# Optimization experiments

Measured on AMD Instinct MI355X. Metric: run time of the kernel, lower is better.

Reference implementation:

```python
import jax, jax.numpy as jnp
import numpy as np

WORDS_CNT = 34835
EMBED_DIM = 512
NEG = -1e30  # stand-in for -inf that is safe under autodiff


def setup_inputs() -> dict:
    key = jax.random.key(0)
    k1, k2, k3, k4, k5 = jax.random.split(key, 5)
    B, Tt, Td = 2048, 30, 150
    title = jax.random.randint(k1, (B, Tt), 0, WORDS_CNT + 1, dtype=jnp.int64)
    desc = jax.random.randint(k2, (B, Td), 0, WORDS_CNT + 1, dtype=jnp.int64)
    t_len = jax.random.randint(k3, (B,), 0, Tt + 1, dtype=jnp.int64)
    d_len = jax.random.randint(k4, (B,), 0, Td + 1, dtype=jnp.int64)
    word2vec = jax.random.normal(k5, (WORDS_CNT + 1, EMBED_DIM), dtype=jnp.float32)
    word2vec = word2vec.at[0].set(0.0)  # padding_idx=0
    return {"title": title, "desc": desc, "t_len": t_len, "d_len": d_len,
            "mode": 0, "word2vec": word2vec}


def _pool(vec, lens):
    # vec: [B, T, D], lens: [B] -> (max_pool [B, D], mean_pool [B, D])
    T = vec.shape[1]
    mask = (jnp.arange(T)[None, :] < lens[:, None])  # [B, T]
    m3 = mask[:, :, None]
    mx = jnp.max(jnp.where(m3, vec, NEG), axis=1)
    nonempty = (lens > 0)[:, None]
    mx = jnp.where(nonempty, mx, 0.0)
    denom = jnp.maximum(lens, 1).astype(vec.dtype)[:, None]
    mean = jnp.sum(jnp.where(m3, vec, 0.0), axis=1) / denom
    mean = jnp.where(nonempty, mean, 0.0)
    return mx, mean


def reference(title, desc, t_len, d_len, mode, word2vec):
    title_vec = word2vec[title]  # [B, Tt, D]
    desc_vec = word2vec[desc]    # [B, Td, D]
    t_max, t_avg = _pool(title_vec, t_len)
    d_max, d_avg = _pool(desc_vec, d_len)
    return jnp.concatenate([t_max, d_max, t_avg, d_avg], axis=1)  # [B, 4*D]
```

## Files before the change

### kernel.cpp

```cpp
#include <hip/hip_runtime.h>

#define TT 30
#define TD 150
#define NEGV -1e30f

__global__ __launch_bounds__(128) void swem_pool_kernel(
    const int* __restrict__ title, const int* __restrict__ desc,
    const int* __restrict__ t_len, const int* __restrict__ d_len,
    const float4* __restrict__ w2v, float4* __restrict__ out)
{
    __shared__ int s_idx[TD];

    const int b   = blockIdx.x;
    const int seg = blockIdx.y;
    const int tid = threadIdx.x;

    const int* toks   = seg ? (desc + b * TD) : (title + b * TT);
    const int  maxlen = seg ? TD : TT;
    const int  len    = seg ? d_len[b] : t_len[b];

    for (int i = tid; i < maxlen; i += 128) s_idx[i] = toks[i];
    __syncthreads();

    float4 mx = make_float4(NEGV, NEGV, NEGV, NEGV);
    float4 sm = make_float4(0.f, 0.f, 0.f, 0.f);

#define ACC(v) \
    mx.x = fmaxf(mx.x, v.x); mx.y = fmaxf(mx.y, v.y); \
    mx.z = fmaxf(mx.z, v.z); mx.w = fmaxf(mx.w, v.w); \
    sm.x += v.x; sm.y += v.y; sm.z += v.z; sm.w += v.w;

    int t = 0;
    for (; t + 8 <= len; t += 8) {
        const float4 v0 = w2v[(size_t)s_idx[t + 0] * 128 + tid];
        const float4 v1 = w2v[(size_t)s_idx[t + 1] * 128 + tid];
        const float4 v2 = w2v[(size_t)s_idx[t + 2] * 128 + tid];
        const float4 v3 = w2v[(size_t)s_idx[t + 3] * 128 + tid];
        const float4 v4 = w2v[(size_t)s_idx[t + 4] * 128 + tid];
        const float4 v5 = w2v[(size_t)s_idx[t + 5] * 128 + tid];
        const float4 v6 = w2v[(size_t)s_idx[t + 6] * 128 + tid];
        const float4 v7 = w2v[(size_t)s_idx[t + 7] * 128 + tid];
        ACC(v0) ACC(v1) ACC(v2) ACC(v3) ACC(v4) ACC(v5) ACC(v6) ACC(v7)
    }
    for (; t < len; ++t) {
        const float4 v = w2v[(size_t)s_idx[t] * 128 + tid];
        ACC(v)
    }
#undef ACC

    float4 rmax, ravg;
    if (len > 0) {
        const float inv = 1.0f / (float)len;
        rmax = mx;
        ravg = make_float4(sm.x * inv, sm.y * inv, sm.z * inv, sm.w * inv);
    } else {
        rmax = make_float4(0.f, 0.f, 0.f, 0.f);
        ravg = make_float4(0.f, 0.f, 0.f, 0.f);
    }

    float4* orow = out + (size_t)b * 512;
    orow[seg * 128 + tid]       = rmax;
    orow[256 + seg * 128 + tid] = ravg;
}

extern "C" void kernel_launch(void* const* d_in, const int* in_sizes, int n_in,
                              void* d_out, int out_size, void* d_ws, size_t ws_size,
                              hipStream_t stream) {
    const int* title = (const int*)d_in[0];
    const int* desc  = (const int*)d_in[1];
    const int* t_len = (const int*)d_in[2];
    const int* d_len = (const int*)d_in[3];
    const float4* w2v = (const float4*)d_in[5];

    float4* out = (float4*)d_out;
    const int B = in_sizes[2];

    dim3 grid(B, 2);
    swem_pool_kernel<<<grid, 128, 0, stream>>>(title, desc, t_len, d_len, w2v, out);
}
```

Baseline: 151.5 us.

## Convert embedding table to fp16 in workspace before gather-pooling

Adds a pre-pass that converts the whole fp32 word2vec table to fp16 in the workspace. The pooling kernel then gathers 8-byte half4 rows and accumulates in fp32, halving the bytes moved by the gather. The trade-off is a full-table read and write on every call plus rounding error from fp16 storage. If the workspace is too small, a non-unrolled fp32 fallback kernel runs instead.

```diff
diff --git a/kernel.cpp b/kernel.cpp
--- a/kernel.cpp
+++ b/kernel.cpp
@@ -1,19 +1,43 @@
 #include <hip/hip_runtime.h>
+#include <hip/hip_fp16.h>
 
 #define TT 30
 #define TD 150
 #define NEGV -1e30f
+#define W2V_ROWS 34836
+#define EMBED 512
 
-__global__ __launch_bounds__(128) void swem_pool_kernel(
+struct __align__(8) Half4 { __half2 a, b; };
+
+__global__ __launch_bounds__(256) void convert_kernel(
+    const float4* __restrict__ src, Half4* __restrict__ dst, int n4)
+{
+    const int stride = gridDim.x * blockDim.x;
+    for (int i = blockIdx.x * blockDim.x + threadIdx.x; i < n4; i += stride) {
+        const float4 v = src[i];
+        Half4 h;
+        h.a = __floats2half2_rn(v.x, v.y);
+        h.b = __floats2half2_rn(v.z, v.w);
+        dst[i] = h;
+    }
+}
+
+#define ACC4(v)                                              \
+    {                                                        \
+        const float2 p = __half22float2((v).a);              \
+        const float2 q = __half22float2((v).b);              \
+        mx.x = fmaxf(mx.x, p.x); mx.y = fmaxf(mx.y, p.y);    \
+        mx.z = fmaxf(mx.z, q.x); mx.w = fmaxf(mx.w, q.y);    \
+        sm.x += p.x; sm.y += p.y; sm.z += q.x; sm.w += q.y;  \
+    }
+
+__global__ __launch_bounds__(128) void swem_pool_h_kernel(
     const int* __restrict__ title, const int* __restrict__ desc,
     const int* __restrict__ t_len, const int* __restrict__ d_len,
-    const float4* __restrict__ w2v, float4* __restrict__ out)
+    const Half4* __restrict__ w2v, float4* __restrict__ out)
 {
     __shared__ int s_idx[TD];
-
-    const int b   = blockIdx.x;
-    const int seg = blockIdx.y;
-    const int tid = threadIdx.x;
+    const int b = blockIdx.x, seg = blockIdx.y, tid = threadIdx.x;
 
     const int* toks   = seg ? (desc + b * TD) : (title + b * TT);
     const int  maxlen = seg ? TD : TT;
@@ -25,28 +49,23 @@
     float4 mx = make_float4(NEGV, NEGV, NEGV, NEGV);
     float4 sm = make_float4(0.f, 0.f, 0.f, 0.f);
 
-#define ACC(v) \
-    mx.x = fmaxf(mx.x, v.x); mx.y = fmaxf(mx.y, v.y); \
-    mx.z = fmaxf(mx.z, v.z); mx.w = fmaxf(mx.w, v.w); \
-    sm.x += v.x; sm.y += v.y; sm.z += v.z; sm.w += v.w;
-
     int t = 0;
     for (; t + 8 <= len; t += 8) {
-        const float4 v0 = w2v[(size_t)s_idx[t + 0] * 128 + tid];
-        const float4 v1 = w2v[(size_t)s_idx[t + 1] * 128 + tid];
-        const float4 v2 = w2v[(size_t)s_idx[t + 2] * 128 + tid];
-        const float4 v3 = w2v[(size_t)s_idx[t + 3] * 128 + tid];
-        const float4 v4 = w2v[(size_t)s_idx[t + 4] * 128 + tid];
-        const float4 v5 = w2v[(size_t)s_idx[t + 5] * 128 + tid];
-        const float4 v6 = w2v[(size_t)s_idx[t + 6] * 128 + tid];
-        const float4 v7 = w2v[(size_t)s_idx[t + 7] * 128 + tid];
-        ACC(v0) ACC(v1) ACC(v2) ACC(v3) ACC(v4) ACC(v5) ACC(v6) ACC(v7)
+        const Half4 v0 = w2v[(size_t)s_idx[t + 0] * 128 + tid];
+        const Half4 v1 = w2v[(size_t)s_idx[t + 1] * 128 + tid];
+        const Half4 v2 = w2v[(size_t)s_idx[t + 2] * 128 + tid];
+        const Half4 v3 = w2v[(size_t)s_idx[t + 3] * 128 + tid];
+        const Half4 v4 = w2v[(size_t)s_idx[t + 4] * 128 + tid];
+        const Half4 v5 = w2v[(size_t)s_idx[t + 5] * 128 + tid];
+        const Half4 v6 = w2v[(size_t)s_idx[t + 6] * 128 + tid];
+        const Half4 v7 = w2v[(size_t)s_idx[t + 7] * 128 + tid];
+        ACC4(v0) ACC4(v1) ACC4(v2) ACC4(v3)
+        ACC4(v4) ACC4(v5) ACC4(v6) ACC4(v7)
     }
     for (; t < len; ++t) {
-        const float4 v = w2v[(size_t)s_idx[t] * 128 + tid];
-        ACC(v)
+        const Half4 v = w2v[(size_t)s_idx[t] * 128 + tid];
+        ACC4(v)
     }
-#undef ACC
 
     float4 rmax, ravg;
     if (len > 0) {
@@ -63,6 +82,41 @@
     orow[256 + seg * 128 + tid] = ravg;
 }
 
+__global__ __launch_bounds__(128) void swem_pool_f_kernel(
+    const int* __restrict__ title, const int* __restrict__ desc,
+    const int* __restrict__ t_len, const int* __restrict__ d_len,
+    const float4* __restrict__ w2v, float4* __restrict__ out)
+{
+    __shared__ int s_idx[TD];
+    const int b = blockIdx.x, seg = blockIdx.y, tid = threadIdx.x;
+    const int* toks   = seg ? (desc + b * TD) : (title + b * TT);
+    const int  maxlen = seg ? TD : TT;
+    const int  len    = seg ? d_len[b] : t_len[b];
+    for (int i = tid; i < maxlen; i += 128) s_idx[i] = toks[i];
+    __syncthreads();
+
+    float4 mx = make_float4(NEGV, NEGV, NEGV, NEGV);
+    float4 sm = make_float4(0.f, 0.f, 0.f, 0.f);
+    for (int t = 0; t < len; ++t) {
+        const float4 v = w2v[(size_t)s_idx[t] * 128 + tid];
+        mx.x = fmaxf(mx.x, v.x); mx.y = fmaxf(mx.y, v.y);
+        mx.z = fmaxf(mx.z, v.z); mx.w = fmaxf(mx.w, v.w);
+        sm.x += v.x; sm.y += v.y; sm.z += v.z; sm.w += v.w;
+    }
+    float4 rmax, ravg;
+    if (len > 0) {
+        const float inv = 1.0f / (float)len;
+        rmax = mx;
+        ravg = make_float4(sm.x * inv, sm.y * inv, sm.z * inv, sm.w * inv);
+    } else {
+        rmax = make_float4(0.f, 0.f, 0.f, 0.f);
+        ravg = make_float4(0.f, 0.f, 0.f, 0.f);
+    }
+    float4* orow = out + (size_t)b * 512;
+    orow[seg * 128 + tid]       = rmax;
+    orow[256 + seg * 128 + tid] = ravg;
+}
+
 extern "C" void kernel_launch(void* const* d_in, const int* in_sizes, int n_in,
                               void* d_out, int out_size, void* d_ws, size_t ws_size,
                               hipStream_t stream) {
@@ -70,11 +124,22 @@
     const int* desc  = (const int*)d_in[1];
     const int* t_len = (const int*)d_in[2];
     const int* d_len = (const int*)d_in[3];
-    const float4* w2v = (const float4*)d_in[5];
+    const float* w2v = (const float*)d_in[5];
 
     float4* out = (float4*)d_out;
     const int B = in_sizes[2];
 
+    const size_t need = (size_t)W2V_ROWS * EMBED * sizeof(__half);
     dim3 grid(B, 2);
-    swem_pool_kernel<<<grid, 128, 0, stream>>>(title, desc, t_len, d_len, w2v, out);
+
+    if (ws_size >= need) {
+        Half4* tab = (Half4*)d_ws;
+        const int n4 = W2V_ROWS * EMBED / 4;
+        convert_kernel<<<4096, 256, 0, stream>>>((const float4*)w2v, tab, n4);
+        swem_pool_h_kernel<<<grid, 128, 0, stream>>>(title, desc, t_len, d_len,
+                                                     tab, out);
+    } else {
+        swem_pool_f_kernel<<<grid, 128, 0, stream>>>(title, desc, t_len, d_len,
+                                                     (const float4*)w2v, out);
+    }
 }
```

Result: faster. 146.1 us (-3.5%).
